# Kernel optimization log

Measured on AMD Instinct MI355X. Metric: run time of the kernel, lower is better.

Reference implementation:

```python
import jax, jax.numpy as jnp
import numpy as np

H, DK = 8, 64  # n_head, d_k = n_feat // n_head
SCALE = 1.0 / np.sqrt(DK)


def setup_inputs() -> dict:
    key0 = jax.random.key(0)
    ks = jax.random.split(key0, 13)
    B, N, T1, T2, F = 16, 4, 256, 1024, 512
    query = jax.random.normal(ks[0], (B, T1, F), jnp.float32)
    key = jax.random.normal(ks[1], (B, N, T2, F), jnp.float32)
    value = jax.random.normal(ks[2], (B, N, T2, F), jnp.float32)
    mask_audio = jax.random.randint(ks[3], (B, N, 1, T2), 0, 2).astype(jnp.int32)
    # guarantee each candidate row has at least one valid key frame
    mask_audio = mask_audio.at[..., 0].set(1)
    mask_spk = jax.random.randint(ks[4], (B, N), 0, 2).astype(jnp.int32)
    # guarantee at least one valid candidate per batch item (avoids all -inf softmax)
    mask_spk = mask_spk.at[:, 0].set(1)
    s = 1.0 / np.sqrt(F)
    Wq = jax.random.normal(ks[5], (F, F), jnp.float32) * s
    bq = jax.random.normal(ks[6], (F,), jnp.float32) * 0.01
    Wk = jax.random.normal(ks[7], (F, F), jnp.float32) * s
    bk = jax.random.normal(ks[8], (F,), jnp.float32) * 0.01
    Wv = jax.random.normal(ks[9], (F, F), jnp.float32) * s
    bv = jax.random.normal(ks[10], (F,), jnp.float32) * 0.01
    Wo = jax.random.normal(ks[11], (F, F), jnp.float32) * s
    bo = jax.random.normal(ks[12], (F,), jnp.float32) * 0.01
    return dict(query=query, key=key, value=value, mask_audio=mask_audio,
                mask_spk=mask_spk, Wq=Wq, bq=bq, Wk=Wk, bk=bk, Wv=Wv, bv=bv,
                Wo=Wo, bo=bo)


def reference(query, key, value, mask_audio, mask_spk, Wq, bq, Wk, bk, Wv, bv, Wo, bo):
    B, T1, F = query.shape
    N, T2 = key.shape[1], key.shape[2]
    # projections (torch Linear: x @ W.T + b)
    q = (query @ Wq.T + bq).reshape(B, T1, H, DK)                 # (B,T1,H,DK)
    k = (key @ Wk.T + bk).reshape(B, N, T2, H, DK)                # (B,N,T2,H,DK)
    v = (value @ Wv.T + bv).reshape(B, N, T2, H, DK)
    # stage 1: intra-candidate temporal attention
    scores = jnp.einsum('bthd,bnshd->bnhts', q, k) * SCALE        # (B,N,H,T1,T2)
    ma = (mask_audio != 0)[:, :, None, :, :]                      # (B,N,1,1,T2)
    scores = jnp.where(ma, scores, -jnp.inf)
    attn1 = jnp.where(ma, jax.nn.softmax(scores, axis=-1), 0.0)
    phone = jnp.einsum('bnhts,bnshd->bnhtd', attn1, v)            # (B,N,H,T1,DK)
    # stage 2: inter-candidate attention
    ss = jnp.einsum('bthd,bnhtd->bthn', q, phone) * SCALE         # (B,T1,H,N)
    ms = (mask_spk != 0)[:, None, None, :]                        # (B,1,1,N)
    ss = jnp.where(ms, ss, -jnp.inf)
    attn2 = jnp.where(ms, jax.nn.softmax(ss, axis=-1), 0.0)
    x = jnp.einsum('bthn,bnhtd->bthd', attn2, phone).reshape(B, T1, H * DK)
    return x @ Wo.T + bo
```

## Files before the change

### kernel.cpp

```cpp
#include <hip/hip_runtime.h>
#include <hip/hip_bf16.h>
#include <math.h>

typedef __attribute__((ext_vector_type(4))) float  f32x4;
typedef __attribute__((ext_vector_type(4))) int    i32x4;
typedef __attribute__((ext_vector_type(8))) __bf16 bf16x8;
typedef __attribute__((ext_vector_type(8))) unsigned short u16x8;
typedef __attribute__((ext_vector_type(4))) unsigned short u16x4;

#define DEV static __device__ __forceinline__

#if __has_builtin(__builtin_amdgcn_permlane32_swap) && __has_builtin(__builtin_amdgcn_permlane16_swap)
#define HAVE_PERMLANE 1
#else
#define HAVE_PERMLANE 0
#endif

namespace {

constexpr int kB = 16, kT1 = 256, kF = 512, kN = 4, kT2 = 1024, kH = 8;
constexpr float kSCALE = 0.125f;
constexpr float kLOG2E = 1.4426950408889634f;

DEV unsigned short f2bf(float f) {
  union { __bf16 h; unsigned short u; } c; c.h = (__bf16)f; return c.u;
}
DEV float bf2f(unsigned short h) {
  union { unsigned u; float f; } c; c.u = ((unsigned)h) << 16;
  return c.f;
}

DEV void async_copy16(const void* g, void* l) {
  __builtin_amdgcn_global_load_lds(
      (const __attribute__((address_space(1))) unsigned int*)g,
      (__attribute__((address_space(3))) unsigned int*)l, 16, 0, 0);
}

DEV bf16x8 cvt8(f32x4 lo, f32x4 hi) {
  bf16x8 r;
  r[0] = (__bf16)lo[0]; r[1] = (__bf16)lo[1]; r[2] = (__bf16)lo[2]; r[3] = (__bf16)lo[3];
  r[4] = (__bf16)hi[0]; r[5] = (__bf16)hi[1]; r[6] = (__bf16)hi[2]; r[7] = (__bf16)hi[3];
  return r;
}

__global__ __launch_bounds__(256) void convert_w(
    const float* __restrict__ w0, const float* __restrict__ w1,
    const float* __restrict__ w2, const float* __restrict__ w3,
    unsigned short* __restrict__ o0, unsigned short* __restrict__ o1,
    unsigned short* __restrict__ o2, unsigned short* __restrict__ o3) {
  const int r = blockIdx.x >> 8;
  const int l = ((blockIdx.x & 255) * 256 + threadIdx.x) * 4;
  const float* src = r == 0 ? w0 : r == 1 ? w1 : r == 2 ? w2 : w3;
  unsigned short* dst = r == 0 ? o0 : r == 1 ? o1 : r == 2 ? o2 : o3;
  const float4 v = *(const float4*)(src + l);
  u16x4 q; q[0] = f2bf(v.x); q[1] = f2bf(v.y); q[2] = f2bf(v.z); q[3] = f2bf(v.w);
  *(u16x4*)(dst + l) = q;
}

template<int MODE>
__global__ __launch_bounds__(512, 2) void gemm256(
    const float* __restrict__ A, const unsigned short* __restrict__ Wb,
    const float* __restrict__ bias, unsigned short* __restrict__ outv) {
  __shared__ __align__(16) unsigned short As[2][256 * 64];
  __shared__ __align__(16) unsigned short Ws[2][256 * 64];
  const int t = threadIdx.x, lane = t & 63, wave = t >> 6;
  const int rb = blockIdx.x >> 1, cb = blockIdx.x & 1;
  const int wr = wave >> 2, wc = wave & 3;
  const int lq = lane & 15, lg = lane >> 4;
  const int arg = t >> 4, as16 = t & 15;

  f32x4 acc[8][4];
#pragma unroll
  for (int i = 0; i < 8; ++i)
#pragma unroll
    for (int j = 0; j < 4; ++j) acc[i][j] = f32x4{0.f, 0.f, 0.f, 0.f};

  f32x4 areg[8];
  bf16x8 af[4][2], bf[4][2];

#define A_ISSUE(kt)                                                             \
  do {                                                                          \
    _Pragma("unroll")                                                           \
    for (int j_ = 0; j_ < 8; ++j_)                                              \
      areg[j_] = *(const f32x4*)(A + (size_t)(rb * 256 + j_ * 32 + arg) * kF +  \
                                 (kt) * 64 + as16 * 4);                         \
  } while (0)

#define A_WRITE(dst)                                                            \
  do {                                                                          \
    _Pragma("unroll")                                                           \
    for (int j_ = 0; j_ < 8; ++j_) {                                            \
      const int row_ = j_ * 32 + arg;                                           \
      const int off_ = row_ * 64 + (((as16 >> 1) ^ (row_ & 7)) << 3) + (as16 & 1) * 4; \
      u16x4 pk_;                                                                \
      pk_[0] = f2bf(areg[j_][0]); pk_[1] = f2bf(areg[j_][1]);                   \
      pk_[2] = f2bf(areg[j_][2]); pk_[3] = f2bf(areg[j_][3]);                   \
      *(u16x4*)&(dst)[off_] = pk_;                                              \
    }                                                                           \
  } while (0)

#define W_ISSUE(kt, dst)                                                        \
  do {                                                                          \
    _Pragma("unroll")                                                           \
    for (int j_ = 0; j_ < 4; ++j_) {                                            \
      const int sidx_ = t + j_ * 512;                                           \
      const int row_ = sidx_ >> 3, s_ = sidx_ & 7;                              \
      async_copy16(Wb + (size_t)(cb * 256 + row_) * kF + (kt) * 64 +            \
                       ((s_ ^ (row_ & 7)) << 3),                                \
                   (dst) + (size_t)(j_ * 512 + wave * 64) * 8);                 \
    }                                                                           \
  } while (0)

#define RD_BF(pw)                                                               \
  do {                                                                          \
    _Pragma("unroll")                                                           \
    for (int n_ = 0; n_ < 4; ++n_) {                                            \
      const int br_ = wc * 64 + n_ * 16 + lq, x7_ = br_ & 7;                    \
      bf[n_][0] = *(const bf16x8*)&(pw)[br_ * 64 + ((lg ^ x7_) << 3)];          \
      bf[n_][1] = *(const bf16x8*)&(pw)[br_ * 64 + (((4 + lg) ^ x7_) << 3)];    \
    }                                                                           \
  } while (0)

#define RD_AF(pa, mb)                                                           \
  do {                                                                          \
    _Pragma("unroll")                                                           \
    for (int m_ = 0; m_ < 4; ++m_) {                                            \
      const int ar_ = wr * 128 + ((mb) + m_) * 16 + lq, x7_ = ar_ & 7;          \
      af[m_][0] = *(const bf16x8*)&(pa)[ar_ * 64 + ((lg ^ x7_) << 3)];          \
      af[m_][1] = *(const bf16x8*)&(pa)[ar_ * 64 + (((4 + lg) ^ x7_) << 3)];    \
    }                                                                           \
  } while (0)

#define MM(mb)                                                                  \
  do {                                                                          \
    _Pragma("unroll")                                                           \
    for (int kk_ = 0; kk_ < 2; ++kk_)                                           \
      _Pragma("unroll")                                                         \
      for (int m_ = 0; m_ < 4; ++m_)                                            \
        _Pragma("unroll")                                                       \
        for (int n_ = 0; n_ < 4; ++n_)                                          \
          acc[(mb) + m_][n_] = __builtin_amdgcn_mfma_f32_16x16x32_bf16(         \
              af[m_][kk_], bf[n_][kk_], acc[(mb) + m_][n_], 0, 0, 0);           \
  } while (0)

#define VMW(n) asm volatile("s_waitcnt vmcnt(" #n ")" ::: "memory")
#define LKW  asm volatile("s_waitcnt lgkmcnt(0)" ::: "memory")
#define SB   __builtin_amdgcn_sched_barrier(0)
#define BAR  do { __builtin_amdgcn_s_barrier(); __builtin_amdgcn_sched_barrier(0); } while (0)

  A_ISSUE(0); W_ISSUE(0, Ws[0]);
  VMW(4); SB;
  A_WRITE(As[0]);
  LKW;

  unsigned short *pa = As[0], *qa = As[1], *pw = Ws[0], *qw = Ws[1];
#pragma unroll 1
  for (int kt = 0; kt < 8; ++kt) {
    if (kt < 7) {
      A_ISSUE(kt + 1);
      W_ISSUE(kt + 1, qw);
      VMW(12); SB;
    } else {
      VMW(0); SB;
    }
    BAR;
    RD_BF(pw); RD_AF(pa, 0);
    LKW; SB;
    __builtin_amdgcn_s_setprio(1); MM(0); __builtin_amdgcn_s_setprio(0); SB;
    RD_AF(pa, 4);
    LKW; SB;
    __builtin_amdgcn_s_setprio(1); MM(4); __builtin_amdgcn_s_setprio(0); SB;
    if (kt < 7) {
      VMW(4); SB;
      A_WRITE(qa);
    }
    LKW; BAR;
    { unsigned short* x = pa; pa = qa; qa = x; }
    { unsigned short* x = pw; pw = qw; qw = x; }
  }

#undef A_ISSUE
#undef A_WRITE
#undef W_ISSUE
#undef RD_BF
#undef RD_AF
#undef MM
#undef VMW
#undef LKW
#undef SB
#undef BAR

  float bs4[4];
#pragma unroll
  for (int n = 0; n < 4; ++n) bs4[n] = bias[cb * 256 + wc * 64 + n * 16 + lq];

#pragma unroll
  for (int m = 0; m < 8; ++m) {
    const int row0 = rb * 256 + wr * 128 + m * 16 + lg * 4;
    const int bn = row0 >> 10, t2 = row0 & 1023;
#pragma unroll
    for (int n = 0; n < 4; ++n) {
      const int col = cb * 256 + wc * 64 + n * 16 + lq;
      const int h = col >> 6, d = col & 63;
      if (MODE == 3) {
        u16x4 pv;
#pragma unroll
        for (int j = 0; j < 4; ++j) pv[j] = f2bf(acc[m][n][j] + bs4[n]);
        *(u16x4*)&outv[(((size_t)(bn * kH + h)) * 64 + d) * kT2 + t2] = pv;
      } else {
#pragma unroll
        for (int j = 0; j < 4; ++j)
          outv[(((size_t)(bn * kH + h)) * kT2 + t2 + j) * 64 + d] =
              f2bf(acc[m][n][j] + bs4[n]);
      }
    }
  }
}

template<int MODE>
__global__ __launch_bounds__(256, 2) void gemm_mixed(
    const float* __restrict__ A, const unsigned short* __restrict__ Wb,
    const float* __restrict__ bias, void* __restrict__ outv, int nrb) {
  __shared__ __align__(16) unsigned short As[2][128 * 64];
  __shared__ __align__(16) unsigned short Bs[3][128 * 64];
  const int t = threadIdx.x, lane = t & 63, wave = t >> 6;
  const int w = blockIdx.x;
  const int xcd = w & 7, s = w >> 3;
  const int rb = xcd * (nrb >> 3) + (s >> 2);
  const int cb = s & 3;
  const int wr = wave >> 1, wc = wave & 1;
  const int lq = lane & 15, lg = lane >> 4;

  const int arow = t >> 1, ah = (t & 1) * 4;
  const float* aptr = A + (size_t)(rb * 128 + arow) * kF + ah * 8;

  f32x4 acc[4][4];
#pragma unroll
  for (int i = 0; i < 4; ++i)
#pragma unroll
    for (int j = 0; j < 4; ++j) acc[i][j] = f32x4{0.f, 0.f, 0.f, 0.f};

  f32x4 arA[8], arB[8];
  bf16x8 af[4][2], bfr[4][2];

#define A_LOAD(kb, ar)                                                          \
  do {                                                                          \
    const f32x4* p_ = (const f32x4*)(aptr + (kb) * 64);                         \
    ar[0]=p_[0]; ar[1]=p_[1]; ar[2]=p_[2]; ar[3]=p_[3];                         \
    ar[4]=p_[4]; ar[5]=p_[5]; ar[6]=p_[6]; ar[7]=p_[7];                         \
  } while (0)

#define A_CVT(ar, dst)                                                          \
  do {                                                                          \
    _Pragma("unroll")                                                           \
    for (int j_ = 0; j_ < 4; ++j_)                                              \
      *(bf16x8*)&(dst)[arow * 64 + (((ah + j_) ^ (arow & 7)) << 3)] =           \
          cvt8(ar[2*j_], ar[2*j_+1]);                                           \
  } while (0)

#define W_STAGE2(kb, dst)                                                       \
  do {                                                                          \
    _Pragma("unroll")                                                           \
    for (int i_ = 0; i_ < 4; ++i_) {                                            \
      const int sidx_ = t + i_ * 256;                                           \
      const int row_ = sidx_ >> 3;                                              \
      const int gseg_ = (sidx_ & 7) ^ (row_ & 7);                               \
      async_copy16(Wb + (size_t)(cb * 128 + row_) * kF + (kb) * 64 + gseg_ * 8, \
                   (dst) + (size_t)(i_ * 256 + wave * 64) * 8);                 \
    }                                                                           \
  } while (0)

#define FRAG(Ap, Wp)                                                            \
  do {                                                                          \
    _Pragma("unroll")                                                           \
    for (int m_ = 0; m_ < 4; ++m_) {                                            \
      const int ar_ = wr * 64 + m_ * 16 + lq, x7_ = ar_ & 7;                    \
      af[m_][0] = *(const bf16x8*)&(Ap)[ar_ * 64 + ((lg       ^ x7_) << 3)];    \
      af[m_][1] = *(const bf16x8*)&(Ap)[ar_ * 64 + (((lg + 4) ^ x7_) << 3)];    \
    }                                                                           \
    _Pragma("unroll")                                                           \
    for (int n_ = 0; n_ < 4; ++n_) {                                            \
      const int br_ = wc * 64 + n_ * 16 + lq, x7_ = br_ & 7;                    \
      bfr[n_][0] = *(const bf16x8*)&(Wp)[br_ * 64 + ((lg       ^ x7_) << 3)];   \
      bfr[n_][1] = *(const bf16x8*)&(Wp)[br_ * 64 + (((lg + 4) ^ x7_) << 3)];   \
    }                                                                           \
  } while (0)

#define MFMA8                                                                   \
  do {                                                                          \
    _Pragma("unroll")                                                           \
    for (int kk_ = 0; kk_ < 2; ++kk_)                                           \
      _Pragma("unroll")                                                         \
      for (int m_ = 0; m_ < 4; ++m_)                                            \
        _Pragma("unroll")                                                       \
        for (int n_ = 0; n_ < 4; ++n_)                                          \
          acc[m_][n_] = __builtin_amdgcn_mfma_f32_16x16x32_bf16(                \
              af[m_][kk_], bfr[n_][kk_], acc[m_][n_], 0, 0, 0);                 \
  } while (0)

#define VMW(n) asm volatile("s_waitcnt vmcnt(" #n ")" ::: "memory")
#define LKW    asm volatile("s_waitcnt lgkmcnt(0)" ::: "memory")
#define BAR    do { __builtin_amdgcn_s_barrier(); __builtin_amdgcn_sched_barrier(0); } while (0)

  A_LOAD(0, arA); A_LOAD(1, arB);
  W_STAGE2(0, Bs[0]); W_STAGE2(1, Bs[1]);
  VMW(16);
  A_CVT(arA, As[0]);
  LKW; BAR;
  A_LOAD(2, arA); W_STAGE2(2, Bs[2]);
  FRAG(As[0], Bs[0]); MFMA8;
  VMW(12); A_CVT(arB, As[1]); LKW; BAR;
  A_LOAD(3, arB); W_STAGE2(3, Bs[0]);
  FRAG(As[1], Bs[1]); MFMA8;
  VMW(12); A_CVT(arA, As[0]); LKW; BAR;
  A_LOAD(4, arA); W_STAGE2(4, Bs[1]);
  FRAG(As[0], Bs[2]); MFMA8;
  VMW(12); A_CVT(arB, As[1]); LKW; BAR;
  A_LOAD(5, arB); W_STAGE2(5, Bs[2]);
  FRAG(As[1], Bs[0]); MFMA8;
  VMW(12); A_CVT(arA, As[0]); LKW; BAR;
  A_LOAD(6, arA); W_STAGE2(6, Bs[0]);
  FRAG(As[0], Bs[1]); MFMA8;
  VMW(12); A_CVT(arB, As[1]); LKW; BAR;
  A_LOAD(7, arB); W_STAGE2(7, Bs[1]);
  FRAG(As[1], Bs[2]); MFMA8;
  VMW(12); A_CVT(arA, As[0]); LKW; BAR;
  FRAG(As[0], Bs[0]); MFMA8;
  VMW(0); A_CVT(arB, As[1]); LKW; BAR;
  FRAG(As[1], Bs[1]); MFMA8;

#undef A_LOAD
#undef A_CVT
#undef W_STAGE2
#undef FRAG
#undef MFMA8
#undef VMW
#undef LKW
#undef BAR

  float bs[4];
#pragma unroll
  for (int n2 = 0; n2 < 4; ++n2) bs[n2] = bias[cb*128 + wc*64 + n2*16 + lq];

#pragma unroll
  for (int m = 0; m < 4; ++m) {
#pragma unroll
    for (int n2 = 0; n2 < 4; ++n2) {
      const int col = cb*128 + wc*64 + n2*16 + lq;
      const int row0 = rb*128 + wr*64 + m*16 + lg*4;
#pragma unroll
      for (int j = 0; j < 4; ++j) {
        const int row = row0 + j;
        const float v = acc[m][n2][j] + bs[n2];
        if (MODE == 2) {
          ((float*)outv)[(size_t)row * kF + col] = v;
        } else {
          const int h = col >> 6, d = col & 63;
          const int b = row >> 8, t1i = row & 255;
          ((unsigned short*)outv)[(((size_t)(b * kH + h)) * kT1 + t1i) * 64 + d] = f2bf(v);
        }
      }
    }
  }
}

__global__ __launch_bounds__(512, 4) void attn_kernel(
    const unsigned short* __restrict__ qh, const unsigned short* __restrict__ kh,
    const unsigned short* __restrict__ vt, const int* __restrict__ mask_audio,
    unsigned short* __restrict__ phone) {
  __shared__ __align__(16) unsigned short Ks[3][64 * 64];
  __shared__ __align__(16) unsigned short Vs[3][64 * 64];
  __shared__ float Mbias[1024];
  const int t = threadIdx.x;
  const int lane = t & 63, wave = t >> 6;
  const int lq = lane & 15, lg = lane >> 4;
  const int w = blockIdx.x;
  const int swz = (w & 7) * 128 + (w >> 3);
  const int qb = swz & 1, bnh = swz >> 1;
  const int h = bnh & 7, n = (bnh >> 3) & 3, b = bnh >> 5;
  const size_t qbase  = ((size_t)(b * kH + h)) * kT1 * 64;
  const size_t kvbase = ((size_t)((b * kN + n) * kH + h)) * kT2 * 64;
  const int* mbase = mask_audio + (size_t)(b * kN + n) * kT2;

  const int srow = (wave << 3) + (lane >> 3);
  const int sgx = ((lane & 7) ^ (srow & 7)) << 3;

#define STAGE_KV(c, kd, vd)                                                       \
  do {                                                                            \
    async_copy16(kh + kvbase + ((size_t)(((c) << 6) + srow) << 6) + sgx,          \
                 (kd) + (wave << 9));                                             \
    async_copy16(vt + kvbase + ((size_t)srow << 10) + ((c) << 6) + sgx,           \
                 (vd) + (wave << 9));                                             \
  } while (0)

  {
    const int i0 = t * 2;
    const int m0 = mbase[i0], m1 = mbase[i0 + 1];
    Mbias[i0]     = m0 ? 0.f : -1e30f;
    Mbias[i0 + 1] = m1 ? 0.f : -1e30f;
  }

  bf16x8 qf0, qf1;
  {
    const unsigned short* qp = qh + qbase +
        ((size_t)((qb << 7) + (wave << 4) + lq) << 6);
    qf0 = *(const bf16x8*)(qp + (lg << 3));
    qf1 = *(const bf16x8*)(qp + 32 + (lg << 3));
  }

  unsigned short *kb0 = Ks[0], *kb1 = Ks[1], *kb2 = Ks[2];
  unsigned short *vb0 = Vs[0], *vb1 = Vs[1], *vb2 = Vs[2];

  STAGE_KV(0, kb0, vb0);
  STAGE_KV(1, kb1, vb1);
  asm volatile("s_waitcnt lgkmcnt(0)" ::: "memory");

  f32x4 of[4];
  float l1 = 0.f;
#pragma unroll
  for (int fd = 0; fd < 4; ++fd) of[fd] = f32x4{0.f, 0.f, 0.f, 0.f};
  const float sc2 = kSCALE * kLOG2E;

#pragma unroll 1
  for (int c = 0; c < 16; ++c) {
    if (c < 15) asm volatile("s_waitcnt vmcnt(2)" ::: "memory");
    else        asm volatile("s_waitcnt vmcnt(0)" ::: "memory");
    __builtin_amdgcn_s_barrier();
    __builtin_amdgcn_sched_barrier(0);

    const float* mrow = Mbias + (c << 6);

    f32x4 sT[4];
#pragma unroll
    for (int kt = 0; kt < 4; ++kt) {
      const int kr = kt * 16 + lq, x7 = kr & 7;
      const bf16x8 kf0 = *(const bf16x8*)&kb0[kr * 64 + ((lg       ^ x7) << 3)];
      const bf16x8 kf1 = *(const bf16x8*)&kb0[kr * 64 + (((lg + 4) ^ x7) << 3)];
      f32x4 sv = f32x4{0.f, 0.f, 0.f, 0.f};
      sv = __builtin_amdgcn_mfma_f32_16x16x32_bf16(kf0, qf0, sv, 0, 0, 0);
      sv = __builtin_amdgcn_mfma_f32_16x16x32_bf16(kf1, qf1, sv, 0, 0, 0);
      sT[kt] = sv;
    }
    float pf[16];
#pragma unroll
    for (int kt = 0; kt < 4; ++kt) {
      const f32x4 mk = *(const f32x4*)&mrow[kt * 16 + lg * 4];
#pragma unroll
      for (int j = 0; j < 4; ++j)
        pf[kt*4+j] = exp2f(fmaf(sT[kt][j], sc2, mk[j]));
    }
    const float a0 = (pf[0] + pf[1]) + (pf[2] + pf[3]);
    const float a1 = (pf[4] + pf[5]) + (pf[6] + pf[7]);
    const float a2 = (pf[8] + pf[9]) + (pf[10] + pf[11]);
    const float a3 = (pf[12] + pf[13]) + (pf[14] + pf[15]);
    l1 += (a0 + a1) + (a2 + a3);
    unsigned pk[8];
#pragma unroll
    for (int kt = 0; kt < 4; ++kt) {
      pk[2*kt]   = (unsigned)f2bf(pf[4*kt+0]) | ((unsigned)f2bf(pf[4*kt+1]) << 16);
      pk[2*kt+1] = (unsigned)f2bf(pf[4*kt+2]) | ((unsigned)f2bf(pf[4*kt+3]) << 16);
    }
    unsigned am0[4], am1[4];
#if HAVE_PERMLANE
    {
      auto x0p = __builtin_amdgcn_permlane32_swap((int)pk[0], (int)pk[2], false, false);
      auto y0p = __builtin_amdgcn_permlane16_swap(x0p[0], x0p[1], false, false);
      am0[0] = (unsigned)y0p[0]; am0[2] = (unsigned)y0p[1];
      auto x1p = __builtin_amdgcn_permlane32_swap((int)pk[1], (int)pk[3], false, false);
      auto y1p = __builtin_amdgcn_permlane16_swap(x1p[0], x1p[1], false, false);
      am0[1] = (unsigned)y1p[0]; am0[3] = (unsigned)y1p[1];
      auto x2p = __builtin_amdgcn_permlane32_swap((int)pk[4], (int)pk[6], false, false);
      auto y2p = __builtin_amdgcn_permlane16_swap(x2p[0], x2p[1], false, false);
      am1[0] = (unsigned)y2p[0]; am1[2] = (unsigned)y2p[1];
      auto x3p = __builtin_amdgcn_permlane32_swap((int)pk[5], (int)pk[7], false, false);
      auto y3p = __builtin_amdgcn_permlane16_swap(x3p[0], x3p[1], false, false);
      am1[1] = (unsigned)y3p[0]; am1[3] = (unsigned)y3p[1];
    }
#else
    {
      const int srcbase = (2 * (lg & 1)) * 16 + lq;
#pragma unroll
      for (int u = 0; u < 4; ++u) {
        const int src = srcbase + (u >> 1) * 16;
        const unsigned va0 = __shfl(pk[(u & 1)],     src);
        const unsigned vb0s = __shfl(pk[2 + (u & 1)], src);
        am0[u] = (lg & 2) ? vb0s : va0;
        const unsigned va1 = __shfl(pk[4 + (u & 1)], src);
        const unsigned vb1s = __shfl(pk[6 + (u & 1)], src);
        am1[u] = (lg & 2) ? vb1s : va1;
      }
    }
#endif
    union { unsigned u[4]; bf16x8 v; } A0, A1;
#pragma unroll
    for (int u = 0; u < 4; ++u) { A0.u[u] = am0[u]; A1.u[u] = am1[u]; }
#pragma unroll
    for (int fd = 0; fd < 4; ++fd) {
      const int d = fd * 16 + lq, x7d = d & 7;
      const bf16x8 vB0 = *(const bf16x8*)&vb0[d * 64 + ((lg       ^ x7d) << 3)];
      const bf16x8 vB1 = *(const bf16x8*)&vb0[d * 64 + (((lg + 4) ^ x7d) << 3)];
      of[fd] = __builtin_amdgcn_mfma_f32_16x16x32_bf16(A0.v, vB0, of[fd], 0, 0, 0);
      of[fd] = __builtin_amdgcn_mfma_f32_16x16x32_bf16(A1.v, vB1, of[fd], 0, 0, 0);
    }

    if (c < 14) STAGE_KV(c + 2, kb2, vb2);
    { unsigned short* x = kb0; kb0 = kb1; kb1 = kb2; kb2 = x; }
    { unsigned short* x = vb0; vb0 = vb1; vb1 = vb2; vb2 = x; }
  }
#undef STAGE_KV

  l1 += __shfl_xor(l1, 16);
  l1 += __shfl_xor(l1, 32);
  const size_t phbase = ((size_t)((b * kN + n) * kH + h)) * kT1 * 64;
  const float li0 = 1.f / __shfl(l1, lg*4 + 0);
  const float li1 = 1.f / __shfl(l1, lg*4 + 1);
  const float li2 = 1.f / __shfl(l1, lg*4 + 2);
  const float li3 = 1.f / __shfl(l1, lg*4 + 3);
#pragma unroll
  for (int fd = 0; fd < 4; ++fd) {
    const int d = fd * 16 + lq;
    const size_t rowb = phbase +
        (size_t)((qb << 7) + (wave << 4) + lg*4) * 64 + d;
    phone[rowb]       = f2bf(of[fd][0] * li0);
    phone[rowb + 64]  = f2bf(of[fd][1] * li1);
    phone[rowb + 128] = f2bf(of[fd][2] * li2);
    phone[rowb + 192] = f2bf(of[fd][3] * li3);
  }
}

__global__ __launch_bounds__(256) void stage2_kernel(
    const unsigned short* __restrict__ qh, const unsigned short* __restrict__ phone,
    const int* __restrict__ mask_spk, float* __restrict__ x) {
  const int t = threadIdx.x, lane = t & 63, wave = t >> 6;
  const int wid = blockIdx.x * 4 + wave;
  const int h = wid & 7;
  const int bt = wid >> 3;
  const int t1i = bt & 255, b = bt >> 8;
  const int d = lane;
  const float q = bf2f(qh[(((size_t)(b * kH + h)) * kT1 + t1i) * 64 + d]);
  float ph[4], ss[4];
#pragma unroll
  for (int n = 0; n < 4; ++n) {
    ph[n] = bf2f(phone[(((size_t)((b * kN + n) * kH + h)) * kT1 + t1i) * 64 + d]);
    float sv = q * ph[n];
#pragma unroll
    for (int o = 1; o < 64; o <<= 1) sv += __shfl_xor(sv, o);
    ss[n] = sv * kSCALE;
  }
  int msk[4];
#pragma unroll
  for (int n = 0; n < 4; ++n) msk[n] = mask_spk[b * kN + n];
  float mx = -INFINITY;
#pragma unroll
  for (int n = 0; n < 4; ++n) if (msk[n]) mx = fmaxf(mx, ss[n]);
  float e[4], sum = 0.f;
#pragma unroll
  for (int n = 0; n < 4; ++n) { const float v = msk[n] ? __expf(ss[n] - mx) : 0.f; e[n] = v; sum += v; }
  float xo = 0.f;
#pragma unroll
  for (int n = 0; n < 4; ++n) xo += e[n] * ph[n];
  xo /= sum;
  x[((size_t)(b * kT1 + t1i)) * kF + h * 64 + d] = xo;
}

}

extern "C" void kernel_launch(void* const* d_in, const int* in_sizes, int n_in,
                              void* d_out, int out_size, void* d_ws, size_t ws_size,
                              hipStream_t stream) {
  (void)in_sizes; (void)n_in; (void)out_size; (void)ws_size;
  const float* query = (const float*)d_in[0];
  const float* key   = (const float*)d_in[1];
  const float* value = (const float*)d_in[2];
  const int* mask_audio = (const int*)d_in[3];
  const int* mask_spk   = (const int*)d_in[4];
  const float* Wq = (const float*)d_in[5];  const float* bq = (const float*)d_in[6];
  const float* Wk = (const float*)d_in[7];  const float* bk = (const float*)d_in[8];
  const float* Wv = (const float*)d_in[9];  const float* bv = (const float*)d_in[10];
  const float* Wo = (const float*)d_in[11]; const float* bo = (const float*)d_in[12];
  float* out = (float*)d_out;

  unsigned short* qws  = (unsigned short*)d_ws;
  unsigned short* kws  = qws  + (size_t)kB * kH * kT1 * 64;
  unsigned short* vws  = kws  + (size_t)kB * kN * kH * kT2 * 64;
  unsigned short* phws = vws  + (size_t)kB * kN * kH * kT2 * 64;
  float*          xws  = (float*)(phws + (size_t)kB * kN * kH * kT1 * 64);
  unsigned short* wqb  = (unsigned short*)(xws + (size_t)kB * kT1 * kF);
  unsigned short* wkb  = wqb + (size_t)kF * kF;
  unsigned short* wvb  = wkb + (size_t)kF * kF;
  unsigned short* wob  = wvb + (size_t)kF * kF;

  convert_w<<<1024, 256, 0, stream>>>(Wq, Wk, Wv, Wo, wqb, wkb, wvb, wob);
  gemm_mixed<0><<<kB * kT1 / 128 * 4, 256, 0, stream>>>(query, wqb, bq, qws, kB * kT1 / 128);
  gemm256<1><<<kB * kN * kT2 / 256 * 2, 512, 0, stream>>>(key,   wkb, bk, kws);
  gemm256<3><<<kB * kN * kT2 / 256 * 2, 512, 0, stream>>>(value, wvb, bv, vws);
  attn_kernel<<<kB * kN * kH * 2, 512, 0, stream>>>(qws, kws, vws, mask_audio, phws);
  stage2_kernel<<<kB * kT1 * kH / 4, 256, 0, stream>>>(qws, phws, mask_spk, xws);
  gemm_mixed<2><<<kB * kT1 / 128 * 4, 256, 0, stream>>>(xws, wob, bo, out, kB * kT1 / 128);
}
```

Measured before the change: 261.4 us.

## Prefetch A two k-tiles ahead with double register buffers and swizzle block order

The projection GEMM now keeps two register buffers for the fp32 A tile and issues global loads two k-steps ahead, fully unrolling the k-loop so the waits can be tuned per step. This is meant to hide global load latency for the A operand behind more MFMA work. It also remaps block indices so consecutive blocks land on different row blocks, which changes cache locality across the grid. The cost is higher register pressure, since a second set of 8 f32x4 registers is live, and that may hurt occupancy under the 512x2 launch bound.

```diff
diff --git a/kernel.cpp b/kernel.cpp
--- a/kernel.cpp
+++ b/kernel.cpp
@@ -64,7 +64,9 @@
   __shared__ __align__(16) unsigned short As[2][256 * 64];
   __shared__ __align__(16) unsigned short Ws[2][256 * 64];
   const int t = threadIdx.x, lane = t & 63, wave = t >> 6;
-  const int rb = blockIdx.x >> 1, cb = blockIdx.x & 1;
+  const int w = blockIdx.x;
+  const int swz = (w & 7) * 64 + (w >> 3);
+  const int rb = swz >> 1, cb = swz & 1;
   const int wr = wave >> 2, wc = wave & 3;
   const int lq = lane & 15, lg = lane >> 4;
   const int arg = t >> 4, as16 = t & 15;
@@ -75,26 +77,26 @@
 #pragma unroll
     for (int j = 0; j < 4; ++j) acc[i][j] = f32x4{0.f, 0.f, 0.f, 0.f};
 
-  f32x4 areg[8];
+  f32x4 arA[8], arB[8];
   bf16x8 af[4][2], bf[4][2];
 
-#define A_ISSUE(kt)                                                             \
+#define A_ISSUE(kt, ar)                                                         \
   do {                                                                          \
     _Pragma("unroll")                                                           \
     for (int j_ = 0; j_ < 8; ++j_)                                              \
-      areg[j_] = *(const f32x4*)(A + (size_t)(rb * 256 + j_ * 32 + arg) * kF +  \
-                                 (kt) * 64 + as16 * 4);                         \
-  } while (0)
-
-#define A_WRITE(dst)                                                            \
+      ar[j_] = *(const f32x4*)(A + (size_t)(rb * 256 + j_ * 32 + arg) * kF +    \
+                               (kt) * 64 + as16 * 4);                           \
+  } while (0)
+
+#define A_WRITE(ar, dst)                                                        \
   do {                                                                          \
     _Pragma("unroll")                                                           \
     for (int j_ = 0; j_ < 8; ++j_) {                                            \
       const int row_ = j_ * 32 + arg;                                           \
       const int off_ = row_ * 64 + (((as16 >> 1) ^ (row_ & 7)) << 3) + (as16 & 1) * 4; \
       u16x4 pk_;                                                                \
-      pk_[0] = f2bf(areg[j_][0]); pk_[1] = f2bf(areg[j_][1]);                   \
-      pk_[2] = f2bf(areg[j_][2]); pk_[3] = f2bf(areg[j_][3]);                   \
+      pk_[0] = f2bf(ar[j_][0]); pk_[1] = f2bf(ar[j_][1]);                       \
+      pk_[2] = f2bf(ar[j_][2]); pk_[3] = f2bf(ar[j_][3]);                       \
       *(u16x4*)&(dst)[off_] = pk_;                                              \
     }                                                                           \
   } while (0)
@@ -148,37 +150,41 @@
 #define SB   __builtin_amdgcn_sched_barrier(0)
 #define BAR  do { __builtin_amdgcn_s_barrier(); __builtin_amdgcn_sched_barrier(0); } while (0)
 
-  A_ISSUE(0); W_ISSUE(0, Ws[0]);
-  VMW(4); SB;
-  A_WRITE(As[0]);
-  LKW;
-
   unsigned short *pa = As[0], *qa = As[1], *pw = Ws[0], *qw = Ws[1];
-#pragma unroll 1
-  for (int kt = 0; kt < 8; ++kt) {
-    if (kt < 7) {
-      A_ISSUE(kt + 1);
-      W_ISSUE(kt + 1, qw);
-      VMW(12); SB;
-    } else {
-      VMW(0); SB;
-    }
-    BAR;
-    RD_BF(pw); RD_AF(pa, 0);
-    LKW; SB;
-    __builtin_amdgcn_s_setprio(1); MM(0); __builtin_amdgcn_s_setprio(0); SB;
-    RD_AF(pa, 4);
-    LKW; SB;
-    __builtin_amdgcn_s_setprio(1); MM(4); __builtin_amdgcn_s_setprio(0); SB;
-    if (kt < 7) {
-      VMW(4); SB;
-      A_WRITE(qa);
-    }
-    LKW; BAR;
-    { unsigned short* x = pa; pa = qa; qa = x; }
-    { unsigned short* x = pw; pw = qw; qw = x; }
-  }
-
+
+  A_ISSUE(0, arA); W_ISSUE(0, pw); A_ISSUE(1, arB);
+  VMW(8); SB;
+  A_WRITE(arA, pa);
+  LKW; BAR;
+
+#define BODY(kt, cur, nxt, WAITN)                                               \
+  do {                                                                          \
+    if ((kt) + 2 < 8) A_ISSUE((kt) + 2, nxt);                                   \
+    if ((kt) + 1 < 8) W_ISSUE((kt) + 1, qw);                                    \
+    VMW(WAITN); SB;              \
+    BAR;                                                                        \
+    RD_BF(pw); RD_AF(pa, 0);                                                    \
+    LKW; SB;                                                                    \
+    __builtin_amdgcn_s_setprio(1); MM(0); __builtin_amdgcn_s_setprio(0); SB;    \
+    RD_AF(pa, 4);                                                               \
+    LKW; SB;                                                                    \
+    __builtin_amdgcn_s_setprio(1); MM(4); __builtin_amdgcn_s_setprio(0); SB;    \
+    if ((kt) + 1 < 8) { A_WRITE(cur, qa); }                                     \
+    LKW; BAR;                                                                   \
+    { unsigned short* x_ = pa; pa = qa; qa = x_; }                              \
+    { unsigned short* x_ = pw; pw = qw; qw = x_; }                              \
+  } while (0)
+
+  BODY(0, arB, arA, 12);
+  BODY(1, arA, arB, 12);
+  BODY(2, arB, arA, 12);
+  BODY(3, arA, arB, 12);
+  BODY(4, arB, arA, 12);
+  BODY(5, arA, arB, 12);
+  BODY(6, arB, arA, 4);
+  BODY(7, arA, arB, 0);
+
+#undef BODY
 #undef A_ISSUE
 #undef A_WRITE
 #undef W_ISSUE
```

After: 392.6 us. +50.2%, slower.

## Halve GEMM K-tile to 32 to raise occupancy, swizzle block order

Applied to the files above, without the earlier changes.

The projection GEMM now stages K in chunks of 32 instead of 64. That halves LDS use per block, so launch bounds go from 2 to 4 blocks per SM. The A/W loads, LDS swizzle patterns and MFMA loops are rewritten for the narrower tile, and the block index is remapped so neighbouring blocks share row or column tiles in cache. The risk is twice as many loop iterations and barriers per output tile, and register pressure from the higher occupancy target.

```diff
diff --git a/kernel.cpp b/kernel.cpp
--- a/kernel.cpp
+++ b/kernel.cpp
@@ -58,16 +58,18 @@
 }
 
 template<int MODE>
-__global__ __launch_bounds__(512, 2) void gemm256(
+__global__ __launch_bounds__(512, 4) void gemm256(
     const float* __restrict__ A, const unsigned short* __restrict__ Wb,
     const float* __restrict__ bias, unsigned short* __restrict__ outv) {
-  __shared__ __align__(16) unsigned short As[2][256 * 64];
-  __shared__ __align__(16) unsigned short Ws[2][256 * 64];
+  __shared__ __align__(16) unsigned short As[2][256 * 32];
+  __shared__ __align__(16) unsigned short Ws[2][256 * 32];
   const int t = threadIdx.x, lane = t & 63, wave = t >> 6;
-  const int rb = blockIdx.x >> 1, cb = blockIdx.x & 1;
+  const int w = blockIdx.x;
+  const int swz = (w & 7) * 64 + (w >> 3);
+  const int rb = swz >> 1, cb = swz & 1;
   const int wr = wave >> 2, wc = wave & 3;
   const int lq = lane & 15, lg = lane >> 4;
-  const int arg = t >> 4, as16 = t & 15;
+  const int arow = t >> 1, ahalf = t & 1;
 
   f32x4 acc[8][4];
 #pragma unroll
@@ -75,72 +77,64 @@
 #pragma unroll
     for (int j = 0; j < 4; ++j) acc[i][j] = f32x4{0.f, 0.f, 0.f, 0.f};
 
-  f32x4 areg[8];
-  bf16x8 af[4][2], bf[4][2];
+  f32x4 areg[4];
+  bf16x8 af[4], bf[4];
 
 #define A_ISSUE(kt)                                                             \
   do {                                                                          \
     _Pragma("unroll")                                                           \
-    for (int j_ = 0; j_ < 8; ++j_)                                              \
-      areg[j_] = *(const f32x4*)(A + (size_t)(rb * 256 + j_ * 32 + arg) * kF +  \
-                                 (kt) * 64 + as16 * 4);                         \
+    for (int j_ = 0; j_ < 4; ++j_)                                              \
+      areg[j_] = *(const f32x4*)(A + (size_t)(rb * 256 + arow) * kF +           \
+                                 (kt) * 32 + ahalf * 16 + j_ * 4);              \
   } while (0)
 
 #define A_WRITE(dst)                                                            \
   do {                                                                          \
-    _Pragma("unroll")                                                           \
-    for (int j_ = 0; j_ < 8; ++j_) {                                            \
-      const int row_ = j_ * 32 + arg;                                           \
-      const int off_ = row_ * 64 + (((as16 >> 1) ^ (row_ & 7)) << 3) + (as16 & 1) * 4; \
-      u16x4 pk_;                                                                \
-      pk_[0] = f2bf(areg[j_][0]); pk_[1] = f2bf(areg[j_][1]);                   \
-      pk_[2] = f2bf(areg[j_][2]); pk_[3] = f2bf(areg[j_][3]);                   \
-      *(u16x4*)&(dst)[off_] = pk_;                                              \
+    const int sw_ = (arow >> 1) & 3;                                            \
+    const int c0_ = (ahalf * 2)     ^ sw_;                                      \
+    const int c1_ = (ahalf * 2 + 1) ^ sw_;                                      \
+    *(bf16x8*)&(dst)[arow * 32 + (c0_ << 3)] = cvt8(areg[0], areg[1]);          \
+    *(bf16x8*)&(dst)[arow * 32 + (c1_ << 3)] = cvt8(areg[2], areg[3]);          \
+  } while (0)
+
+#define W_ISSUE(kt, dst)                                                        \
+  do {                                                                          \
+    _Pragma("unroll")                                                           \
+    for (int j_ = 0; j_ < 2; ++j_) {                                            \
+      const int sidx_ = t + j_ * 512;                                           \
+      const int row_ = sidx_ >> 2, c_ = sidx_ & 3;                              \
+      async_copy16(Wb + (size_t)(cb * 256 + row_) * kF + (kt) * 32 +            \
+                       ((c_ ^ ((row_ >> 1) & 3)) << 3),                         \
+                   (dst) + (size_t)sidx_ * 8);                                  \
     }                                                                           \
   } while (0)
 
-#define W_ISSUE(kt, dst)                                                        \
-  do {                                                                          \
-    _Pragma("unroll")                                                           \
-    for (int j_ = 0; j_ < 4; ++j_) {                                            \
-      const int sidx_ = t + j_ * 512;                                           \
-      const int row_ = sidx_ >> 3, s_ = sidx_ & 7;                              \
-      async_copy16(Wb + (size_t)(cb * 256 + row_) * kF + (kt) * 64 +            \
-                       ((s_ ^ (row_ & 7)) << 3),                                \
-                   (dst) + (size_t)(j_ * 512 + wave * 64) * 8);                 \
+#define RD_BF(pw)                                                               \
+  do {                                                                          \
+    _Pragma("unroll")                                                           \
+    for (int n_ = 0; n_ < 4; ++n_) {                                            \
+      const int br_ = wc * 64 + n_ * 16 + lq;                                   \
+      bf[n_] = *(const bf16x8*)&(pw)[br_ * 32 + ((lg ^ ((br_ >> 1) & 3)) << 3)];\
     }                                                                           \
   } while (0)
 
-#define RD_BF(pw)                                                               \
-  do {                                                                          \
-    _Pragma("unroll")                                                           \
-    for (int n_ = 0; n_ < 4; ++n_) {                                            \
-      const int br_ = wc * 64 + n_ * 16 + lq, x7_ = br_ & 7;                    \
-      bf[n_][0] = *(const bf16x8*)&(pw)[br_ * 64 + ((lg ^ x7_) << 3)];          \
-      bf[n_][1] = *(const bf16x8*)&(pw)[br_ * 64 + (((4 + lg) ^ x7_) << 3)];    \
+#define RD_AF(pa, mb)                                                           \
+  do {                                                                          \
+    _Pragma("unroll")                                                           \
+    for (int m_ = 0; m_ < 4; ++m_) {                                            \
+      const int ar_ = wr * 128 + ((mb) + m_) * 16 + lq;                         \
+      af[m_] = *(const bf16x8*)&(pa)[ar_ * 32 + ((lg ^ ((ar_ >> 1) & 3)) << 3)];\
     }                                                                           \
   } while (0)
 
-#define RD_AF(pa, mb)                                                           \
-  do {                                                                          \
-    _Pragma("unroll")                                                           \
-    for (int m_ = 0; m_ < 4; ++m_) {                                            \
-      const int ar_ = wr * 128 + ((mb) + m_) * 16 + lq, x7_ = ar_ & 7;          \
-      af[m_][0] = *(const bf16x8*)&(pa)[ar_ * 64 + ((lg ^ x7_) << 3)];          \
-      af[m_][1] = *(const bf16x8*)&(pa)[ar_ * 64 + (((4 + lg) ^ x7_) << 3)];    \
-    }                                                                           \
-  } while (0)
-
 #define MM(mb)                                                                  \
   do {                                                                          \
     _Pragma("unroll")                                                           \
-    for (int kk_ = 0; kk_ < 2; ++kk_)                                           \
+    for (int m_ = 0; m_ < 4; ++m_)                                              \
       _Pragma("unroll")                                                         \
-      for (int m_ = 0; m_ < 4; ++m_)                                            \
-        _Pragma("unroll")                                                       \
-        for (int n_ = 0; n_ < 4; ++n_)                                          \
-          acc[(mb) + m_][n_] = __builtin_amdgcn_mfma_f32_16x16x32_bf16(         \
-              af[m_][kk_], bf[n_][kk_], acc[(mb) + m_][n_], 0, 0, 0);           \
+      for (int n_ = 0; n_ < 4; ++n_)                                            \
+        acc[(mb) + m_][n_] = __builtin_amdgcn_mfma_f32_16x16x32_bf16(           \
+            af[m_], bf[n_], acc[(mb) + m_][n_], 0, 0, 0);                       \
   } while (0)
 
 #define VMW(n) asm volatile("s_waitcnt vmcnt(" #n ")" ::: "memory")
@@ -148,18 +142,19 @@
 #define SB   __builtin_amdgcn_sched_barrier(0)
 #define BAR  do { __builtin_amdgcn_s_barrier(); __builtin_amdgcn_sched_barrier(0); } while (0)
 
-  A_ISSUE(0); W_ISSUE(0, Ws[0]);
-  VMW(4); SB;
-  A_WRITE(As[0]);
+  unsigned short *pa = As[0], *qa = As[1], *pw = Ws[0], *qw = Ws[1];
+
+  A_ISSUE(0); W_ISSUE(0, pw);
+  VMW(2); SB;
+  A_WRITE(pa);
   LKW;
 
-  unsigned short *pa = As[0], *qa = As[1], *pw = Ws[0], *qw = Ws[1];
 #pragma unroll 1
-  for (int kt = 0; kt < 8; ++kt) {
-    if (kt < 7) {
+  for (int kt = 0; kt < 16; ++kt) {
+    if (kt < 15) {
       A_ISSUE(kt + 1);
       W_ISSUE(kt + 1, qw);
-      VMW(12); SB;
+      VMW(6); SB;
     } else {
       VMW(0); SB;
     }
@@ -170,8 +165,8 @@
     RD_AF(pa, 4);
     LKW; SB;
     __builtin_amdgcn_s_setprio(1); MM(4); __builtin_amdgcn_s_setprio(0); SB;
-    if (kt < 7) {
-      VMW(4); SB;
+    if (kt < 15) {
+      VMW(2); SB;
       A_WRITE(qa);
     }
     LKW; BAR;
```

Result: slower. 938.3 us (+258.9%).
